# Optimization experiments

Measured on AMD Instinct MI355X. Metric: run time of the kernel, lower is better.

## Reference

```python
import jax, jax.numpy as jnp
import numpy as np

B, IN_DIM, N_NODES, N_LEAVES, N_ACTIONS = 131072, 128, 511, 512, 16


def setup_inputs() -> dict:
    key = jax.random.key(0)
    k1, k2, k3, k4 = jax.random.split(key, 4)
    x = jax.random.normal(k1, (B, IN_DIM), dtype=jnp.float32)
    W1 = jax.random.normal(k2, (N_NODES, IN_DIM), dtype=jnp.float32) * 0.1
    b1 = jax.random.normal(k3, (N_NODES,), dtype=jnp.float32) * 0.1
    W2 = jax.random.normal(k4, (N_LEAVES, 2 * N_NODES), dtype=jnp.float32) * 0.05
    # leaf -> action assignment; arange % n_actions guarantees every group non-empty
    leaf_actions = (jnp.arange(N_LEAVES) % N_ACTIONS).astype(jnp.int32)
    return {"x": x, "W1": W1, "b1": b1, "W2": W2, "leaf_actions": leaf_actions}


def reference(x, W1, b1, W2, leaf_actions):
    # linear1
    h = x @ W1.T + b1                      # [B, N_NODES]
    # relu(h) || relu(-h)
    z = jnp.concatenate([jax.nn.relu(h), jax.nn.relu(-h)], axis=1)  # [B, 2*N_NODES]
    # linear2 (no bias)
    y = z @ W2.T                           # [B, N_LEAVES]
    # grouped segment-max over leaf columns, grouped by action id
    pooled = jax.ops.segment_max(y.T, leaf_actions, num_segments=N_ACTIONS).T  # [B, N_ACTIONS]
    return jax.nn.softmax(pooled, axis=-1)
```

## Files before the change

### kernel.cpp

```cpp
#include <hip/hip_runtime.h>
#include <hip/hip_bf16.h>

typedef unsigned short u16;
typedef unsigned int u32;
typedef __attribute__((ext_vector_type(8))) short bf16x8;
typedef __attribute__((ext_vector_type(16))) float f32x16;

#define NROWS   131072
#define KDIM    128
#define NNODES  511
#define NACT    16

__device__ __forceinline__ u16 f2b(float v) {
  return __builtin_bit_cast(u16, __float2bfloat16(v));
}

union Frag {
  bf16x8 v;
  u16    u[8];
  int4   i;
  int    d[4];
};

#define Z16 {0.f,0.f,0.f,0.f,0.f,0.f,0.f,0.f,0.f,0.f,0.f,0.f,0.f,0.f,0.f,0.f}

__global__ void prep_k(const float* __restrict__ W1, const float* __restrict__ W2,
                       const float* __restrict__ b1, u16* __restrict__ w1f,
                       u16* __restrict__ wgt, float* __restrict__ b1r) {
  int bid = blockIdx.x, t = threadIdx.x;
  if (bid < 256) {
    int o = bid * 256 + t;
    int j = o & 7, l = (o >> 3) & 63, ks = (o >> 9) & 7, nt = o >> 12;
    int node = nt * 32 + (l & 31);
    int k = ks * 16 + ((l >> 5) << 3) + j;
    w1f[o] = f2b(node < NNODES ? W1[node * KDIM + k] : 0.f);
  } else if (bid < 2304) {
    int o = (bid - 256) * 256 + t;
    int j = o & 7, l = (o >> 3) & 63, lt = (o >> 9) & 15, s = o >> 13;
    int type = s & 1, kstep = s >> 1;
    int leaf = lt * 32 + (l & 31);
    int n = kstep * 16 + ((l >> 5) << 3) + j;
    float va = 0.f, vb = 0.f;
    if (n < NNODES) {
      va = W2[leaf * (2 * NNODES) + n];
      vb = W2[leaf * (2 * NNODES) + NNODES + n];
    }
    wgt[o] = f2b(type ? 0.5f * (va + vb) : 0.5f * (va - vb));
  } else {
    int o = (bid - 2304) * 256 + t;
    int r = o & 15, hi2 = (o >> 4) & 1, nt = o >> 5;
    int node = nt * 32 + (r & 3) + 8 * (r >> 2) + 4 * hi2;
    b1r[o] = (node < NNODES) ? b1[node] : 0.f;
  }
}

__global__ __launch_bounds__(1024, 4) void fused_k(const float* __restrict__ x,
                                                   const u16* __restrict__ w1f,
                                                   const u16* __restrict__ wgt,
                                                   const float* __restrict__ b1r,
                                                   float* __restrict__ out) {
  __shared__ u16 Hh[4 * 32 * 64 * 8];
  __shared__ u16 Ss[32 * 64 * 8];

  const int t = threadIdx.x, w = t >> 6, l = t & 63;
  const int la = l & 31, hi = l >> 5;
  const int rg = blockIdx.x;

  {
    const float* xb = x + (size_t)rg * 128 * KDIM;
#pragma unroll
    for (int i = 0; i < 2; ++i) {
      int f = w * 2 + i;
      int rt = f >> 3, ks = f & 7;
      const float* src = xb + (rt * 32 + la) * KDIM + ks * 16 + hi * 8;
      float4 v0 = *(const float4*)src;
      float4 v1 = *(const float4*)(src + 4);
      Frag fr;
      fr.u[0] = f2b(v0.x); fr.u[1] = f2b(v0.y); fr.u[2] = f2b(v0.z); fr.u[3] = f2b(v0.w);
      fr.u[4] = f2b(v1.x); fr.u[5] = f2b(v1.y); fr.u[6] = f2b(v1.z); fr.u[7] = f2b(v1.w);
      *(int4*)&Ss[f * 512 + l * 8] = fr.i;
    }
  }
  __syncthreads();

  {
    Frag a1[8];
#pragma unroll
    for (int q = 0; q < 8; ++q)
      a1[q].i = *(const int4*)(w1f + ((size_t)(w * 8 + q) * 64 + l) * 8);
    float4 bias[4];
#pragma unroll
    for (int g = 0; g < 4; ++g)
      bias[g] = *(const float4*)(b1r + (w * 2 + hi) * 16 + g * 4);

#pragma unroll 1
    for (int rt = 0; rt < 4; ++rt) {
      f32x16 c0 = Z16;
#pragma unroll
      for (int ks = 0; ks < 8; ++ks) {
        Frag b;
        b.i = *(const int4*)&Ss[(rt * 8 + ks) * 512 + l * 8];
        c0 = __builtin_amdgcn_mfma_f32_32x32x16_bf16(a1[ks].v, b.v, c0, 0, 0, 0);
      }
#pragma unroll
      for (int p = 0; p < 8; ++p) {
        int q = p >> 1, e = p & 1;
        int r0 = 4 * q + 2 * e;
        float bv0 = e ? bias[q].z : bias[q].x;
        float bv1 = e ? bias[q].w : bias[q].y;
        float v0 = c0[r0] + bv0;
        float v1 = c0[r0 + 1] + bv1;
        int n32 = 8 * q + 4 * hi + 2 * e;
        int c_h = n32 >> 4, jj = n32 & 15;
        u32 pkv = (u32)f2b(v0) | ((u32)f2b(v1) << 16);
        *(u32*)&Hh[((rt * 32 + w * 2 + c_h) * 64 + ((jj >> 3) << 5) + la) * 8 + (jj & 6)] = pkv;
      }
    }
  }
  __syncthreads();

  f32x16 acc[4] = {Z16, Z16, Z16, Z16};

#define WADDR(k, type) (wgt + ((size_t)((k) * 32 + (type) * 16 + w)) * 512 + l * 8)

  Frag AD, AS, BD, BS;
  AD.i = *(const int4*)WADDR(0, 0); AS.i = *(const int4*)WADDR(0, 1);
  BD.i = *(const int4*)WADDR(1, 0); BS.i = *(const int4*)WADDR(1, 1);

#define KSTEP(kk, D, S, kpf)                                                              \
  {                                                                                       \
    Frag ha[4];                                                                           \
    _Pragma("unroll") for (int rt = 0; rt < 4; ++rt)                                      \
      ha[rt].i = *(const int4*)&Hh[((rt * 32 + (kk)) * 64 + l) * 8];                      \
    _Pragma("unroll") for (int rt = 0; rt < 4; ++rt)                                      \
      acc[rt] = __builtin_amdgcn_mfma_f32_32x32x16_bf16(ha[rt].v, D.v, acc[rt], 0, 0, 0); \
    _Pragma("unroll") for (int rt = 0; rt < 4; ++rt)                                      \
      _Pragma("unroll") for (int d = 0; d < 4; ++d) ha[rt].d[d] &= 0x7FFF7FFF;            \
    _Pragma("unroll") for (int rt = 0; rt < 4; ++rt)                                      \
      acc[rt] = __builtin_amdgcn_mfma_f32_32x32x16_bf16(ha[rt].v, S.v, acc[rt], 0, 0, 0); \
    if ((kpf) < 32) {                                                                     \
      D.i = *(const int4*)WADDR((kpf), 0);                                                \
      S.i = *(const int4*)WADDR((kpf), 1);                                                \
    }                                                                                     \
  }

#pragma unroll 1
  for (int k = 0; k < 32; k += 2) {
    KSTEP(k,     AD, AS, k + 2);
    KSTEP(k + 1, BD, BS, k + 3);
  }

  __syncthreads();

  float* Hred = (float*)Hh;
#pragma unroll
  for (int rt = 0; rt < 4; ++rt)
#pragma unroll
    for (int r = 0; r < 16; ++r) {
      float v = acc[rt][r];
      v = fmaxf(v, __shfl_xor(v, 16));
      int row = rt * 32 + (r & 3) + 8 * (r >> 2) + 4 * hi;
      if (la < 16) Hred[(w * 128 + row) * 16 + la] = v;
    }
  __syncthreads();
  {
    int row = t >> 3, ap = t & 7;
    float m0 = -1e30f, m1 = -1e30f;
#pragma unroll
    for (int ww = 0; ww < 16; ++ww) {
      m0 = fmaxf(m0, Hred[(ww * 128 + row) * 16 + ap]);
      m1 = fmaxf(m1, Hred[(ww * 128 + row) * 16 + ap + 8]);
    }
    float m = fmaxf(m0, m1);
    m = fmaxf(m, __shfl_xor(m, 1));
    m = fmaxf(m, __shfl_xor(m, 2));
    m = fmaxf(m, __shfl_xor(m, 4));
    float e0 = __expf(m0 - m), e1 = __expf(m1 - m);
    float s = e0 + e1;
    s += __shfl_xor(s, 1);
    s += __shfl_xor(s, 2);
    s += __shfl_xor(s, 4);
    float inv = 1.f / s;
    float* orow = out + ((size_t)rg * 128 + row) * NACT;
    orow[ap]     = e0 * inv;
    orow[ap + 8] = e1 * inv;
  }
}

extern "C" void kernel_launch(void* const* d_in, const int* in_sizes, int n_in,
                              void* d_out, int out_size, void* d_ws, size_t ws_size,
                              hipStream_t stream) {
  const float* x  = (const float*)d_in[0];
  const float* W1 = (const float*)d_in[1];
  const float* b1 = (const float*)d_in[2];
  const float* W2 = (const float*)d_in[3];

  char* ws = (char*)d_ws;
  u16*   w1f = (u16*)ws;
  u16*   wgt = (u16*)(ws + 131072);
  float* b1r = (float*)(ws + 131072 + 1048576);

  prep_k <<<dim3(2308), dim3(256), 0, stream>>>(W1, W2, b1, w1f, wgt, b1r);
  fused_k<<<dim3(NROWS / 128), dim3(1024), 0, stream>>>(x, w1f, wgt, b1r, (float*)d_out);
}
```

Measured before the change: 250.6 us.

## Swizzle H tile in LDS and software-pipeline H fragment reads across k-steps

Applies an XOR swizzle (lane ^ lane>>3) to the LDS layout of the hidden activations, on both the write in stage one and the read in stage two, to reduce bank conflicts. The second-stage MFMA loop is also restructured so the H fragments for the next k-step are loaded from LDS while the current MFMAs issue, hiding LDS latency. This raises register pressure, with more live fragments under a 1024-thread, 4-waves-per-SIMD launch bound, which could cause spills.

Result: no change. 246.9 us (-1.5%).

```diff
diff --git a/kernel.cpp b/kernel.cpp
--- a/kernel.cpp
+++ b/kernel.cpp
@@ -113,41 +113,51 @@
         int n32 = 8 * q + 4 * hi + 2 * e;
         int c_h = n32 >> 4, jj = n32 & 15;
         u32 pkv = (u32)f2b(v0) | ((u32)f2b(v1) << 16);
-        *(u32*)&Hh[((rt * 32 + w * 2 + c_h) * 64 + ((jj >> 3) << 5) + la) * 8 + (jj & 6)] = pkv;
+        int lam = ((jj >> 3) << 5) + la;
+        int sb2 = lam ^ (lam >> 3);
+        *(u32*)&Hh[((rt * 32 + w * 2 + c_h) * 64 + sb2) * 8 + (jj & 6)] = pkv;
       }
     }
   }
   __syncthreads();
 
   f32x16 acc[4] = {Z16, Z16, Z16, Z16};
-
+  const int sl = l ^ (l >> 3);
+
+#define RDH(kk, rt) (*(const int4*)&Hh[(((rt) * 32 + (kk)) * 64 + sl) * 8])
 #define WADDR(k, type) (wgt + ((size_t)((k) * 32 + (type) * 16 + w)) * 512 + l * 8)
-
-  Frag AD, AS, BD, BS;
+#define ABS4(F) { _Pragma("unroll") for (int d = 0; d < 4; ++d) (F).d[d] &= 0x7FFF7FFF; }
+#define MF(A, B, r) acc[r] = __builtin_amdgcn_mfma_f32_32x32x16_bf16((A).v, (B).v, acc[r], 0, 0, 0)
+
+  Frag X0, X1, Y0, Y1, C2, C3, AD, AS, BD, BS;
+  X0.i = RDH(0, 0); X1.i = RDH(0, 1);
   AD.i = *(const int4*)WADDR(0, 0); AS.i = *(const int4*)WADDR(0, 1);
   BD.i = *(const int4*)WADDR(1, 0); BS.i = *(const int4*)WADDR(1, 1);
 
-#define KSTEP(kk, D, S, kpf)                                                              \
-  {                                                                                       \
-    Frag ha[4];                                                                           \
-    _Pragma("unroll") for (int rt = 0; rt < 4; ++rt)                                      \
-      ha[rt].i = *(const int4*)&Hh[((rt * 32 + (kk)) * 64 + l) * 8];                      \
-    _Pragma("unroll") for (int rt = 0; rt < 4; ++rt)                                      \
-      acc[rt] = __builtin_amdgcn_mfma_f32_32x32x16_bf16(ha[rt].v, D.v, acc[rt], 0, 0, 0); \
-    _Pragma("unroll") for (int rt = 0; rt < 4; ++rt)                                      \
-      _Pragma("unroll") for (int d = 0; d < 4; ++d) ha[rt].d[d] &= 0x7FFF7FFF;            \
-    _Pragma("unroll") for (int rt = 0; rt < 4; ++rt)                                      \
-      acc[rt] = __builtin_amdgcn_mfma_f32_32x32x16_bf16(ha[rt].v, S.v, acc[rt], 0, 0, 0); \
-    if ((kpf) < 32) {                                                                     \
-      D.i = *(const int4*)WADDR((kpf), 0);                                                \
-      S.i = *(const int4*)WADDR((kpf), 1);                                                \
-    }                                                                                     \
-  }
-
 #pragma unroll 1
   for (int k = 0; k < 32; k += 2) {
-    KSTEP(k,     AD, AS, k + 2);
-    KSTEP(k + 1, BD, BS, k + 3);
+    C2.i = RDH(k, 2); C3.i = RDH(k, 3);
+    Y0.i = RDH(k + 1, 0); Y1.i = RDH(k + 1, 1);
+    MF(X0, AD, 0); MF(X1, AD, 1);
+    MF(C2, AD, 2); MF(C3, AD, 3);
+    ABS4(X0); ABS4(X1); ABS4(C2); ABS4(C3);
+    MF(X0, AS, 0); MF(X1, AS, 1);
+    MF(C2, AS, 2); MF(C3, AS, 3);
+    if (k + 2 < 32) {
+      AD.i = *(const int4*)WADDR(k + 2, 0);
+      AS.i = *(const int4*)WADDR(k + 2, 1);
+    }
+    C2.i = RDH(k + 1, 2); C3.i = RDH(k + 1, 3);
+    if (k + 2 < 32) { X0.i = RDH(k + 2, 0); X1.i = RDH(k + 2, 1); }
+    MF(Y0, BD, 0); MF(Y1, BD, 1);
+    MF(C2, BD, 2); MF(C3, BD, 3);
+    ABS4(Y0); ABS4(Y1); ABS4(C2); ABS4(C3);
+    MF(Y0, BS, 0); MF(Y1, BS, 1);
+    MF(C2, BS, 2); MF(C3, BS, 3);
+    if (k + 3 < 32) {
+      BD.i = *(const int4*)WADDR(k + 3, 0);
+      BS.i = *(const int4*)WADDR(k + 3, 1);
+    }
   }
 
   __syncthreads();
```

## Halve rows per block and give each wave two leaf tiles

Applied to the files above, without the earlier changes.

The fused kernel now processes 64 rows per 512-thread block instead of 128 rows per 1024-thread block. Each wave computes two layer-1 node tiles, then a 2x2 (row tile x leaf tile) layer-2 tile so each H fragment feeds two weight fragments. The shared-memory footprint per block is halved, which can let more blocks share a CU and overlap the staging, GEMM and reduction phases. The segment-max reduction buffer gets an XOR swizzle to reduce bank conflicts. The cost is that the full W2 weight stream is read twice as often per row from L2, and each wave needs more registers for weight fragments.

Result: faster. 244.2 us (-2.5%).

```diff
diff --git a/kernel.cpp b/kernel.cpp
--- a/kernel.cpp
+++ b/kernel.cpp
@@ -54,20 +54,20 @@
   }
 }
 
-__global__ __launch_bounds__(1024, 4) void fused_k(const float* __restrict__ x,
-                                                   const u16* __restrict__ w1f,
-                                                   const u16* __restrict__ wgt,
-                                                   const float* __restrict__ b1r,
-                                                   float* __restrict__ out) {
-  __shared__ u16 Hh[4 * 32 * 64 * 8];
-  __shared__ u16 Ss[32 * 64 * 8];
+__global__ __launch_bounds__(512, 4) void fused_k(const float* __restrict__ x,
+                                                  const u16* __restrict__ w1f,
+                                                  const u16* __restrict__ wgt,
+                                                  const float* __restrict__ b1r,
+                                                  float* __restrict__ out) {
+  __shared__ u16 Hh[2 * 32 * 64 * 8];
+  __shared__ u16 Ss[16 * 64 * 8];
 
   const int t = threadIdx.x, w = t >> 6, l = t & 63;
   const int la = l & 31, hi = l >> 5;
   const int rg = blockIdx.x;
 
   {
-    const float* xb = x + (size_t)rg * 128 * KDIM;
+    const float* xb = x + (size_t)rg * 64 * KDIM;
 #pragma unroll
     for (int i = 0; i < 2; ++i) {
       int f = w * 2 + i;
@@ -83,18 +83,20 @@
   }
   __syncthreads();
 
-  {
+#pragma unroll 1
+  for (int nn = 0; nn < 2; ++nn) {
+    const int nt = w * 2 + nn;
     Frag a1[8];
 #pragma unroll
     for (int q = 0; q < 8; ++q)
-      a1[q].i = *(const int4*)(w1f + ((size_t)(w * 8 + q) * 64 + l) * 8);
+      a1[q].i = *(const int4*)(w1f + ((size_t)(nt * 8 + q) * 64 + l) * 8);
     float4 bias[4];
 #pragma unroll
     for (int g = 0; g < 4; ++g)
-      bias[g] = *(const float4*)(b1r + (w * 2 + hi) * 16 + g * 4);
+      bias[g] = *(const float4*)(b1r + (nt * 2 + hi) * 16 + g * 4);
 
 #pragma unroll 1
-    for (int rt = 0; rt < 4; ++rt) {
+    for (int rt = 0; rt < 2; ++rt) {
       f32x16 c0 = Z16;
 #pragma unroll
       for (int ks = 0; ks < 8; ++ks) {
@@ -113,63 +115,72 @@
         int n32 = 8 * q + 4 * hi + 2 * e;
         int c_h = n32 >> 4, jj = n32 & 15;
         u32 pkv = (u32)f2b(v0) | ((u32)f2b(v1) << 16);
-        *(u32*)&Hh[((rt * 32 + w * 2 + c_h) * 64 + ((jj >> 3) << 5) + la) * 8 + (jj & 6)] = pkv;
+        *(u32*)&Hh[((rt * 32 + nt * 2 + c_h) * 64 + ((jj >> 3) << 5) + la) * 8 + (jj & 6)] = pkv;
       }
     }
   }
   __syncthreads();
 
-  f32x16 acc[4] = {Z16, Z16, Z16, Z16};
-
-#define WADDR(k, type) (wgt + ((size_t)((k) * 32 + (type) * 16 + w)) * 512 + l * 8)
-
-  Frag AD, AS, BD, BS;
-  AD.i = *(const int4*)WADDR(0, 0); AS.i = *(const int4*)WADDR(0, 1);
-  BD.i = *(const int4*)WADDR(1, 0); BS.i = *(const int4*)WADDR(1, 1);
-
-#define KSTEP(kk, D, S, kpf)                                                              \
-  {                                                                                       \
-    Frag ha[4];                                                                           \
-    _Pragma("unroll") for (int rt = 0; rt < 4; ++rt)                                      \
-      ha[rt].i = *(const int4*)&Hh[((rt * 32 + (kk)) * 64 + l) * 8];                      \
-    _Pragma("unroll") for (int rt = 0; rt < 4; ++rt)                                      \
-      acc[rt] = __builtin_amdgcn_mfma_f32_32x32x16_bf16(ha[rt].v, D.v, acc[rt], 0, 0, 0); \
-    _Pragma("unroll") for (int rt = 0; rt < 4; ++rt)                                      \
-      _Pragma("unroll") for (int d = 0; d < 4; ++d) ha[rt].d[d] &= 0x7FFF7FFF;            \
-    _Pragma("unroll") for (int rt = 0; rt < 4; ++rt)                                      \
-      acc[rt] = __builtin_amdgcn_mfma_f32_32x32x16_bf16(ha[rt].v, S.v, acc[rt], 0, 0, 0); \
-    if ((kpf) < 32) {                                                                     \
-      D.i = *(const int4*)WADDR((kpf), 0);                                                \
-      S.i = *(const int4*)WADDR((kpf), 1);                                                \
-    }                                                                                     \
+  f32x16 acc[2][2] = {{Z16, Z16}, {Z16, Z16}};
+
+#define WADDR(k, type, i) (wgt + ((size_t)((k) * 32 + (type) * 16 + w * 2 + (i))) * 512 + l * 8)
+
+  Frag Ad0, Ad1, As0, As1, Bd0, Bd1, Bs0, Bs1;
+  Ad0.i = *(const int4*)WADDR(0, 0, 0); Ad1.i = *(const int4*)WADDR(0, 0, 1);
+  As0.i = *(const int4*)WADDR(0, 1, 0); As1.i = *(const int4*)WADDR(0, 1, 1);
+  Bd0.i = *(const int4*)WADDR(1, 0, 0); Bd1.i = *(const int4*)WADDR(1, 0, 1);
+  Bs0.i = *(const int4*)WADDR(1, 1, 0); Bs1.i = *(const int4*)WADDR(1, 1, 1);
+
+#define KSTEP(kk, D0, D1, S0, S1, kpf)                                                            \
+  {                                                                                               \
+    Frag ha[2];                                                                                   \
+    _Pragma("unroll") for (int rt = 0; rt < 2; ++rt)                                              \
+      ha[rt].i = *(const int4*)&Hh[((rt * 32 + (kk)) * 64 + l) * 8];                              \
+    _Pragma("unroll") for (int rt = 0; rt < 2; ++rt) {                                            \
+      acc[rt][0] = __builtin_amdgcn_mfma_f32_32x32x16_bf16(ha[rt].v, D0.v, acc[rt][0], 0, 0, 0);  \
+      acc[rt][1] = __builtin_amdgcn_mfma_f32_32x32x16_bf16(ha[rt].v, D1.v, acc[rt][1], 0, 0, 0);  \
+    }                                                                                             \
+    _Pragma("unroll") for (int rt = 0; rt < 2; ++rt)                                              \
+      _Pragma("unroll") for (int d = 0; d < 4; ++d) ha[rt].d[d] &= 0x7FFF7FFF;                    \
+    _Pragma("unroll") for (int rt = 0; rt < 2; ++rt) {                                            \
+      acc[rt][0] = __builtin_amdgcn_mfma_f32_32x32x16_bf16(ha[rt].v, S0.v, acc[rt][0], 0, 0, 0);  \
+      acc[rt][1] = __builtin_amdgcn_mfma_f32_32x32x16_bf16(ha[rt].v, S1.v, acc[rt][1], 0, 0, 0);  \
+    }                                                                                             \
+    if ((kpf) < 32) {                                                                             \
+      D0.i = *(const int4*)WADDR((kpf), 0, 0); D1.i = *(const int4*)WADDR((kpf), 0, 1);           \
+      S0.i = *(const int4*)WADDR((kpf), 1, 0); S1.i = *(const int4*)WADDR((kpf), 1, 1);           \
+    }                                                                                             \
   }
 
 #pragma unroll 1
   for (int k = 0; k < 32; k += 2) {
-    KSTEP(k,     AD, AS, k + 2);
-    KSTEP(k + 1, BD, BS, k + 3);
-  }
+    KSTEP(k,     Ad0, Ad1, As0, As1, k + 2);
+    KSTEP(k + 1, Bd0, Bd1, Bs0, Bs1, k + 3);
+  }
+#undef KSTEP
+#undef WADDR
 
   __syncthreads();
 
   float* Hred = (float*)Hh;
 #pragma unroll
-  for (int rt = 0; rt < 4; ++rt)
+  for (int rt = 0; rt < 2; ++rt)
 #pragma unroll
     for (int r = 0; r < 16; ++r) {
-      float v = acc[rt][r];
+      int row = rt * 32 + (r & 3) + 8 * (r >> 2) + 4 * hi;
+      float v = fmaxf(acc[rt][0][r], acc[rt][1][r]);
       v = fmaxf(v, __shfl_xor(v, 16));
-      int row = rt * 32 + (r & 3) + 8 * (r >> 2) + 4 * hi;
-      if (la < 16) Hred[(w * 128 + row) * 16 + la] = v;
+      Hred[(w * 64 + row) * 32 + (la ^ ((r & 3) << 2))] = v;
     }
   __syncthreads();
   {
     int row = t >> 3, ap = t & 7;
+    int xr = (row & 3) << 2;
     float m0 = -1e30f, m1 = -1e30f;
 #pragma unroll
-    for (int ww = 0; ww < 16; ++ww) {
-      m0 = fmaxf(m0, Hred[(ww * 128 + row) * 16 + ap]);
-      m1 = fmaxf(m1, Hred[(ww * 128 + row) * 16 + ap + 8]);
+    for (int ww = 0; ww < 8; ++ww) {
+      m0 = fmaxf(m0, Hred[(ww * 64 + row) * 32 + (ap ^ xr)]);
+      m1 = fmaxf(m1, Hred[(ww * 64 + row) * 32 + (((ap + 8) ^ xr) & 15)]);
     }
     float m = fmaxf(m0, m1);
     m = fmaxf(m, __shfl_xor(m, 1));
@@ -181,7 +192,7 @@
     s += __shfl_xor(s, 2);
     s += __shfl_xor(s, 4);
     float inv = 1.f / s;
-    float* orow = out + ((size_t)rg * 128 + row) * NACT;
+    float* orow = out + ((size_t)rg * 64 + row) * NACT;
     orow[ap]     = e0 * inv;
     orow[ap + 8] = e1 * inv;
   }
@@ -201,5 +212,5 @@
   float* b1r = (float*)(ws + 131072 + 1048576);
 
   prep_k <<<dim3(2308), dim3(256), 0, stream>>>(W1, W2, b1, w1f, wgt, b1r);
-  fused_k<<<dim3(NROWS / 128), dim3(1024), 0, stream>>>(x, w1f, wgt, b1r, (float*)d_out);
-}
+  fused_k<<<dim3(NROWS / 64), dim3(512), 0, stream>>>(x, w1f, wgt, b1r, (float*)d_out);
+}
```
